# Performance work log

Measured on AMD Instinct MI355X. Metric: run time of the kernel, lower is better.

The kernel has to match this reference:

```python
import jax, jax.numpy as jnp
import numpy as np

N, L = 1, 384
NODE, H, PD = 256, 8, 128
HD = NODE // H
D1 = H * PD + NODE  # out_transform input dim = 1280


def instance_norm(x, eps=1e-5):
    # x: (N, C, H, W); torch InstanceNorm2d default: no affine, biased var
    m = x.mean(axis=(2, 3), keepdims=True)
    v = x.var(axis=(2, 3), keepdims=True)
    return (x - m) / jnp.sqrt(v + eps)


def conv3x3(x, w, b):
    y = jax.lax.conv_general_dilated(x, w, (1, 1), 'SAME',
                                     dimension_numbers=('NCHW', 'OIHW', 'NCHW'))
    return y + b[None, :, None, None]


def leaky(x):
    return jnp.where(x >= 0, x, 0.01 * x)


def layer_norm(x, w, b, eps=1e-5):
    m = x.mean(-1, keepdims=True)
    v = x.var(-1, keepdims=True)
    return (x - m) / jnp.sqrt(v + eps) * w + b


def setup_inputs() -> dict:
    key = jax.random.key(0)
    ks = jax.random.split(key, 32)
    s = 0.05
    inp = {
        'x': jax.random.normal(ks[0], (N, L, NODE), jnp.float32),
        'z': jax.random.normal(ks[1], (N, L, L, PD), jnp.float32),
        'plddt': jax.random.uniform(ks[2], (N, L, L, 1), jnp.float32),
        # linear weights stored (in, out) so application is x @ W
        'Wq': jax.random.normal(ks[3], (NODE, NODE), jnp.float32) * s,
        'Wk': jax.random.normal(ks[4], (NODE, NODE), jnp.float32) * s,
        'Wv': jax.random.normal(ks[5], (NODE, NODE), jnp.float32) * s,
        'Wp2a': jax.random.normal(ks[6], (PD, H), jnp.float32) * s,
        'conv_a_w': jax.random.normal(ks[7], (H, 2 * H, 3, 3), jnp.float32) * s,
        'conv_a_b': jnp.zeros((H,), jnp.float32),
        'conv_m_w': jax.random.normal(ks[8], (H, H + 1, 3, 3), jnp.float32) * s,
        'conv_m_b': jnp.zeros((H,), jnp.float32),
        'ln1_w': jnp.ones((D1,), jnp.float32),
        'ln1_b': jnp.zeros((D1,), jnp.float32),
        'lin1_w': jax.random.normal(ks[9], (D1, 2 * NODE), jnp.float32) * s,
        'lin1_b': jnp.zeros((2 * NODE,), jnp.float32),
        'ln2_w': jnp.ones((2 * NODE,), jnp.float32),
        'ln2_b': jnp.zeros((2 * NODE,), jnp.float32),
        'lin2_w': jax.random.normal(ks[10], (2 * NODE, NODE), jnp.float32) * s,
        'lin2_b': jnp.zeros((NODE,), jnp.float32),
        'lnf_w': jnp.ones((NODE,), jnp.float32),
        'lnf_b': jnp.zeros((NODE,), jnp.float32),
        'conv_p_w': jax.random.normal(ks[11], (PD, H + PD, 3, 3), jnp.float32) * s,
        'conv_p_b': jnp.zeros((PD,), jnp.float32),
    }
    return inp


def reference(x, z, plddt, Wq, Wk, Wv, Wp2a, conv_a_w, conv_a_b, conv_m_w,
              conv_m_b, ln1_w, ln1_b, lin1_w, lin1_b, ln2_w, ln2_b, lin2_w,
              lin2_b, lnf_w, lnf_b, conv_p_w, conv_p_b):
    Nb, Lh, D = x.shape
    nh = conv_a_w.shape[0]
    hd = D // nh
    Pd = z.shape[-1]
    # node -> alpha (GAT-style QK scores per head)
    q = (x @ Wq).reshape(Nb, Lh, nh, hd)
    k = (x @ Wk).reshape(Nb, Lh, nh, hd)
    v = (x @ Wv).reshape(Nb, Lh, nh, hd)
    a_node = jnp.einsum('nlhd,nmhd->nlmh', q, k) / jnp.sqrt(jnp.float32(hd))
    a_pair = z @ Wp2a                                  # (N,L,L,H)
    a = jnp.concatenate([a_pair, a_node], -1).transpose(0, 3, 1, 2)  # (N,2H,L,L)
    a = leaky(conv3x3(instance_norm(a), conv_a_w, conv_a_b))
    a = jnp.concatenate([a, plddt.transpose(0, 3, 1, 2)], 1)          # (N,H+1,L,L)
    a = leaky(conv3x3(instance_norm(a), conv_m_w, conv_m_b))
    a = a.transpose(0, 2, 3, 1)                                        # (N,L,L,H)
    # aggregations
    nfn = jnp.einsum('nlmh,nmhd->nlhd', a, v).reshape(Nb, Lh, D)       # node from node
    nfp = jnp.einsum('nlmh,nlmp->nlhp', a, z).reshape(Nb, Lh, nh * Pd) # node from pair
    cat = jnp.concatenate([nfp, nfn], -1)
    h = layer_norm(cat, ln1_w, ln1_b) @ lin1_w + lin1_b
    h = leaky(layer_norm(h, ln2_w, ln2_b)) @ lin2_w + lin2_b
    x_new = layer_norm(x + h, lnf_w, lnf_b)
    zp = jnp.concatenate([z, a], -1).transpose(0, 3, 1, 2)             # (N,P+H,L,L)
    z_new = leaky(conv3x3(instance_norm(zp), conv_p_w, conv_p_b)).transpose(0, 2, 3, 1)
    return x_new, z_new
```

## Files before the change

kernel.cpp:

```cpp
#include <hip/hip_runtime.h>
#include <stdint.h>

#define LSEQ 384
#define LL   147456
#define NODE 256
#define NH   8
#define HD   32
#define PDIM 128
#define D1   1280
#define D2   512

typedef __attribute__((ext_vector_type(8))) short s16x8;
typedef __attribute__((ext_vector_type(8))) __bf16 bf16x8;
typedef __attribute__((ext_vector_type(4))) float f32x4;

__device__ __forceinline__ float bf2f(uint16_t u) {
    union { uint32_t i; float f; } x; x.i = ((uint32_t)u) << 16; return x.f;
}
__device__ __forceinline__ uint16_t f2bf(float f) {
    uint32_t b = __float_as_uint(f);
    return (uint16_t)((b + 0x7FFFu + ((b >> 16) & 1u)) >> 16);
}
__device__ __forceinline__ float ld(const void* p, size_t i, int bf) {
    return bf ? bf2f(((const uint16_t*)p)[i]) : ((const float*)p)[i];
}
__device__ __forceinline__ void stout(void* p, size_t i, float v, int bf) {
    if (bf) ((uint16_t*)p)[i] = f2bf(v);
    else    ((float*)p)[i] = v;
}

__device__ __forceinline__ bf16x8 bf16x8_zero() {
    union { s16x8 s; bf16x8 b; } u; u.s = (s16x8)0; return u.b;
}

__device__ __forceinline__ void block_reduce2_256(float* s1, float* s2, int t) {
    __syncthreads();
    for (int o = 128; o > 0; o >>= 1) {
        if (t < o) { s1[t] += s1[t + o]; s2[t] += s2[t + o]; }
        __syncthreads();
    }
}

__device__ __forceinline__ void acc8(uint4 u, float& s, float& ss) {
    uint32_t w[4] = { u.x, u.y, u.z, u.w };
    #pragma unroll
    for (int i = 0; i < 4; ++i) {
        float a = bf2f((uint16_t)(w[i] & 0xFFFFu));
        float b = bf2f((uint16_t)(w[i] >> 16));
        s += a + b;
        ss = fmaf(a, a, ss);
        ss = fmaf(b, b, ss);
    }
}

__global__ void k_detect(const uint32_t* __restrict__ zz, int* __restrict__ flag) {
    if (threadIdx.x == 0 && blockIdx.x == 0) {
        int cnt = 0;
        for (int i = 0; i < 256; ++i) {
            uint32_t lo = zz[i] & 0xFFFFu;
            uint32_t e = (lo >> 7) & 0xFFu;
            if (lo == 0u || (e >= 96u && e <= 142u)) ++cnt;
        }
        flag[0] = (cnt >= 192) ? 1 : 0;
    }
}

__global__ __launch_bounds__(256) void k_cvt(
    const void* __restrict__ src, uint16_t* __restrict__ dst, const int* __restrict__ dt)
{
    int bf = dt[0];
    int i = blockIdx.x * 256 + threadIdx.x;
    dst[i] = f2bf(ld(src, i, bf));
}

__global__ __launch_bounds__(256) void k_wnk(
    const void* __restrict__ src, uint16_t* __restrict__ dst, int K, int N,
    const int* __restrict__ dt)
{
    __shared__ float tile[32][33];
    int bf = dt[0];
    int k0 = blockIdx.x * 32, n0 = blockIdx.y * 32;
    int tr = threadIdx.x >> 5, tc = threadIdx.x & 31;
    #pragma unroll
    for (int i = 0; i < 4; ++i)
        tile[tr + i * 8][tc] = ld(src, (size_t)(k0 + tr + i * 8) * N + n0 + tc, bf);
    __syncthreads();
    #pragma unroll
    for (int i = 0; i < 4; ++i)
        dst[(size_t)(n0 + tr + i * 8) * K + k0 + tc] = f2bf(tile[tc][tr + i * 8]);
}

__global__ __launch_bounds__(256) void k_gemm_bias_f32(
    const uint16_t* __restrict__ A, const uint16_t* __restrict__ B,
    const void* __restrict__ bias, float* __restrict__ out, int K, int N,
    const int* __restrict__ dt)
{
    __shared__ __align__(16) uint16_t As[64 * 72];
    __shared__ __align__(16) uint16_t Bs[64 * 72];
    int bf = dt[0];
    int t = threadIdx.x;
    int row0 = blockIdx.x * 64, col0 = blockIdx.y * 64;
    int w = t >> 6, lane = t & 63, p = lane & 15, g = lane >> 4;
    int wm = w >> 1, wn = w & 1;
    f32x4 acc[2][2];
    #pragma unroll
    for (int i = 0; i < 2; ++i)
        #pragma unroll
        for (int j = 0; j < 2; ++j) acc[i][j] = (f32x4){0.f, 0.f, 0.f, 0.f};

    for (int kc = 0; kc < K; kc += 64) {
        __syncthreads();
        #pragma unroll
        for (int rep = 0; rep < 2; ++rep) {
            int i = t + rep * 256;
            int r = i >> 3, c8 = (i & 7) * 8;
            *(uint4*)&As[r * 72 + c8] = *(const uint4*)&A[(size_t)(row0 + r) * K + kc + c8];
            *(uint4*)&Bs[r * 72 + c8] = *(const uint4*)&B[(size_t)(col0 + r) * K + kc + c8];
        }
        __syncthreads();
        #pragma unroll
        for (int kk = 0; kk < 64; kk += 32) {
            bf16x8 a0 = *(const bf16x8*)&As[(wm * 32 + p) * 72 + kk + 8 * g];
            bf16x8 a1 = *(const bf16x8*)&As[(wm * 32 + 16 + p) * 72 + kk + 8 * g];
            bf16x8 b0 = *(const bf16x8*)&Bs[(wn * 32 + p) * 72 + kk + 8 * g];
            bf16x8 b1 = *(const bf16x8*)&Bs[(wn * 32 + 16 + p) * 72 + kk + 8 * g];
            acc[0][0] = __builtin_amdgcn_mfma_f32_16x16x32_bf16(a0, b0, acc[0][0], 0, 0, 0);
            acc[0][1] = __builtin_amdgcn_mfma_f32_16x16x32_bf16(a0, b1, acc[0][1], 0, 0, 0);
            acc[1][0] = __builtin_amdgcn_mfma_f32_16x16x32_bf16(a1, b0, acc[1][0], 0, 0, 0);
            acc[1][1] = __builtin_amdgcn_mfma_f32_16x16x32_bf16(a1, b1, acc[1][1], 0, 0, 0);
        }
    }
    #pragma unroll
    for (int mi = 0; mi < 2; ++mi)
        #pragma unroll
        for (int ni = 0; ni < 2; ++ni) {
            int n = col0 + wn * 32 + ni * 16 + p;
            float bb = ld(bias, n, bf);
            #pragma unroll
            for (int reg = 0; reg < 4; ++reg) {
                int m = row0 + wm * 32 + mi * 16 + 4 * g + reg;
                out[(size_t)m * N + n] = acc[mi][ni][reg] + bb;
            }
        }
}

__global__ __launch_bounds__(256) void k_gemm_qkv(
    const uint16_t* __restrict__ A, const uint16_t* __restrict__ B,
    uint16_t* __restrict__ q, uint16_t* __restrict__ k, uint16_t* __restrict__ v)
{
    __shared__ __align__(16) uint16_t As[64 * 72];
    __shared__ __align__(16) uint16_t Bs[64 * 72];
    const int K = 256;
    int t = threadIdx.x;
    int row0 = blockIdx.x * 64, col0 = blockIdx.y * 64;
    int w = t >> 6, lane = t & 63, p = lane & 15, g = lane >> 4;
    int wm = w >> 1, wn = w & 1;
    f32x4 acc[2][2];
    #pragma unroll
    for (int i = 0; i < 2; ++i)
        #pragma unroll
        for (int j = 0; j < 2; ++j) acc[i][j] = (f32x4){0.f, 0.f, 0.f, 0.f};

    for (int kc = 0; kc < K; kc += 64) {
        __syncthreads();
        #pragma unroll
        for (int rep = 0; rep < 2; ++rep) {
            int i = t + rep * 256;
            int r = i >> 3, c8 = (i & 7) * 8;
            *(uint4*)&As[r * 72 + c8] = *(const uint4*)&A[(size_t)(row0 + r) * K + kc + c8];
            *(uint4*)&Bs[r * 72 + c8] = *(const uint4*)&B[(size_t)(col0 + r) * K + kc + c8];
        }
        __syncthreads();
        #pragma unroll
        for (int kk = 0; kk < 64; kk += 32) {
            bf16x8 a0 = *(const bf16x8*)&As[(wm * 32 + p) * 72 + kk + 8 * g];
            bf16x8 a1 = *(const bf16x8*)&As[(wm * 32 + 16 + p) * 72 + kk + 8 * g];
            bf16x8 b0 = *(const bf16x8*)&Bs[(wn * 32 + p) * 72 + kk + 8 * g];
            bf16x8 b1 = *(const bf16x8*)&Bs[(wn * 32 + 16 + p) * 72 + kk + 8 * g];
            acc[0][0] = __builtin_amdgcn_mfma_f32_16x16x32_bf16(a0, b0, acc[0][0], 0, 0, 0);
            acc[0][1] = __builtin_amdgcn_mfma_f32_16x16x32_bf16(a0, b1, acc[0][1], 0, 0, 0);
            acc[1][0] = __builtin_amdgcn_mfma_f32_16x16x32_bf16(a1, b0, acc[1][0], 0, 0, 0);
            acc[1][1] = __builtin_amdgcn_mfma_f32_16x16x32_bf16(a1, b1, acc[1][1], 0, 0, 0);
        }
    }
    #pragma unroll
    for (int mi = 0; mi < 2; ++mi)
        #pragma unroll
        for (int ni = 0; ni < 2; ++ni) {
            int nglob = col0 + wn * 32 + ni * 16 + p;
            int sel = nglob >> 8, col = nglob & 255;
            uint16_t* dst = (sel == 0) ? q : (sel == 1) ? k : v;
            #pragma unroll
            for (int reg = 0; reg < 4; ++reg) {
                int m = row0 + wm * 32 + mi * 16 + 4 * g + reg;
                dst[(size_t)m * 256 + col] = f2bf(acc[mi][ni][reg]);
            }
        }
}

__global__ __launch_bounds__(256) void k_lin2lnf_mfma(
    const uint16_t* __restrict__ A, const uint16_t* __restrict__ B,
    const void* __restrict__ bias, const void* __restrict__ x,
    const void* __restrict__ lnw, const void* __restrict__ lnb,
    void* __restrict__ out, const int* __restrict__ dt)
{
    __shared__ __align__(16) uint16_t As[32 * 72];
    __shared__ __align__(16) uint16_t Bs[256 * 72];
    const int K = 512;
    int bf = dt[0];
    int t = threadIdx.x;
    int row0 = blockIdx.x * 32;
    int w = t >> 6, lane = t & 63, p = lane & 15, g = lane >> 4;
    f32x4 acc[2][4];
    #pragma unroll
    for (int i = 0; i < 2; ++i)
        #pragma unroll
        for (int j = 0; j < 4; ++j) acc[i][j] = (f32x4){0.f, 0.f, 0.f, 0.f};

    for (int kc = 0; kc < K; kc += 64) {
        __syncthreads();
        {
            int r = t >> 3, c8 = (t & 7) * 8;
            *(uint4*)&As[r * 72 + c8] = *(const uint4*)&A[(size_t)(row0 + r) * K + kc + c8];
        }
        #pragma unroll
        for (int rep = 0; rep < 8; ++rep) {
            int i = t + rep * 256;
            int r = i >> 3, c8 = (i & 7) * 8;
            *(uint4*)&Bs[r * 72 + c8] = *(const uint4*)&B[(size_t)r * K + kc + c8];
        }
        __syncthreads();
        #pragma unroll
        for (int kk = 0; kk < 64; kk += 32) {
            bf16x8 a0 = *(const bf16x8*)&As[(p) * 72 + kk + 8 * g];
            bf16x8 a1 = *(const bf16x8*)&As[(16 + p) * 72 + kk + 8 * g];
            #pragma unroll
            for (int ni = 0; ni < 4; ++ni) {
                bf16x8 bq = *(const bf16x8*)&Bs[(w * 64 + ni * 16 + p) * 72 + kk + 8 * g];
                acc[0][ni] = __builtin_amdgcn_mfma_f32_16x16x32_bf16(a0, bq, acc[0][ni], 0, 0, 0);
                acc[1][ni] = __builtin_amdgcn_mfma_f32_16x16x32_bf16(a1, bq, acc[1][ni], 0, 0, 0);
            }
        }
    }
    __syncthreads();
    float* lnt = (float*)Bs;
    #pragma unroll
    for (int mi = 0; mi < 2; ++mi)
        #pragma unroll
        for (int ni = 0; ni < 4; ++ni) {
            int n = w * 64 + ni * 16 + p;
            float bb = ld(bias, n, bf);
            #pragma unroll
            for (int reg = 0; reg < 4; ++reg) {
                int m = mi * 16 + 4 * g + reg;
                lnt[m * 264 + n] = acc[mi][ni][reg] + bb + ld(x, (size_t)(row0 + m) * 256 + n, bf);
            }
        }
    __syncthreads();
    for (int rr = 0; rr < 8; ++rr) {
        int m = w * 8 + rr;
        float4 v4 = *(const float4*)&lnt[m * 264 + lane * 4];
        float vv[4] = { v4.x, v4.y, v4.z, v4.w };
        float s = (vv[0] + vv[1]) + (vv[2] + vv[3]);
        float ss = fmaf(vv[0], vv[0], fmaf(vv[1], vv[1], fmaf(vv[2], vv[2], vv[3] * vv[3])));
        #pragma unroll
        for (int off = 32; off > 0; off >>= 1) {
            s  += __shfl_xor(s, off);
            ss += __shfl_xor(ss, off);
        }
        float mean = s / 256.f;
        float rstd = rsqrtf(fmaxf(ss / 256.f - mean * mean, 0.f) + 1e-5f);
        #pragma unroll
        for (int i = 0; i < 4; ++i) {
            int c = lane * 4 + i;
            float val = (vv[i] - mean) * rstd * ld(lnw, c, bf) + ld(lnb, c, bf);
            stout(out, (size_t)(row0 + m) * 256 + c, val, bf);
        }
    }
}

__global__ __launch_bounds__(256) void k_apair(
    const void* __restrict__ z, const void* __restrict__ Wp2a,
    uint16_t* __restrict__ acat, const int* __restrict__ dt)
{
    __shared__ float zl[32 * 129];
    __shared__ float wp[PDIM * NH];
    int bf = dt[0];
    int t = threadIdx.x, m0 = blockIdx.x * 32, l = blockIdx.y;
    for (int i = t; i < PDIM * NH; i += 256) wp[i] = ld(Wp2a, i, bf);
    if (bf) {
        const uint16_t* zz = (const uint16_t*)z;
        for (int grp = t; grp < 512; grp += 256) {
            int ml = grp >> 4, p8 = (grp & 15) * 8;
            uint4 u = *(const uint4*)&zz[((size_t)(l * LSEQ + m0 + ml)) * PDIM + p8];
            const uint16_t* pu = (const uint16_t*)&u;
            #pragma unroll
            for (int j = 0; j < 8; ++j) zl[ml * 129 + p8 + j] = bf2f(pu[j]);
        }
    } else {
        const float* zz = (const float*)z;
        for (int grp = t; grp < 1024; grp += 256) {
            int ml = grp >> 5, p4 = (grp & 31) * 4;
            float4 u = *(const float4*)&zz[((size_t)(l * LSEQ + m0 + ml)) * PDIM + p4];
            zl[ml * 129 + p4 + 0] = u.x; zl[ml * 129 + p4 + 1] = u.y;
            zl[ml * 129 + p4 + 2] = u.z; zl[ml * 129 + p4 + 3] = u.w;
        }
    }
    __syncthreads();
    int h = t >> 5, ml = t & 31;
    float acc = 0.f;
    for (int p = 0; p < PDIM; ++p) acc = fmaf(zl[ml * 129 + p], wp[p * NH + h], acc);
    acat[(size_t)h * LL + l * LSEQ + m0 + ml] = f2bf(acc);
}

__global__ __launch_bounds__(256) void k_anode(
    const uint16_t* __restrict__ q, const uint16_t* __restrict__ k,
    uint16_t* __restrict__ acat)
{
    __shared__ float kl[NODE * 33];
    __shared__ float qr[NH * 33];
    int t = threadIdx.x, m0 = blockIdx.x * 32, l = blockIdx.y;
    for (int grp = t; grp < 1024; grp += 256) {
        int ml = grp >> 5, c8 = (grp & 31) * 8;
        uint4 u = *(const uint4*)&k[(size_t)(m0 + ml) * NODE + c8];
        const uint16_t* pu = (const uint16_t*)&u;
        #pragma unroll
        for (int j = 0; j < 8; ++j) kl[(c8 + j) * 33 + ml] = bf2f(pu[j]);
    }
    qr[(t >> 5) * 33 + (t & 31)] = bf2f(q[l * NODE + t]);
    __syncthreads();
    int h = t >> 5, ml = t & 31;
    float acc = 0.f;
    #pragma unroll 8
    for (int d = 0; d < HD; ++d)
        acc = fmaf(qr[h * 33 + d], kl[(h * HD + d) * 33 + ml], acc);
    acat[(size_t)(NH + h) * LL + l * LSEQ + m0 + ml] = f2bf(acc * 0.17677669529663687f);
}

__global__ __launch_bounds__(256) void k_scp(
    const uint16_t* __restrict__ src, const void* __restrict__ raw,
    float* __restrict__ ps, float* __restrict__ pss, const int* __restrict__ dt, int C)
{
    __shared__ float s1[256], s2[256];
    int c = blockIdx.y, chunk = blockIdx.x, t = threadIdx.x;
    float s = 0.f, ss = 0.f;
    if (c < C) {
        const uint16_t* p = src + (size_t)c * LL + (size_t)chunk * 8192;
        #pragma unroll
        for (int it = 0; it < 4; ++it) acc8(*(const uint4*)&p[(it * 256 + t) * 8], s, ss);
    } else if (dt[0]) {
        const uint4* p = (const uint4*)raw + (size_t)chunk * 1024;
        #pragma unroll
        for (int it = 0; it < 4; ++it) acc8(p[it * 256 + t], s, ss);
    } else {
        const float4* p = (const float4*)raw + (size_t)chunk * 2048;
        #pragma unroll
        for (int it = 0; it < 8; ++it) {
            float4 a = p[it * 256 + t];
            s += (a.x + a.y) + (a.z + a.w);
            ss = fmaf(a.x, a.x, fmaf(a.y, a.y, fmaf(a.z, a.z, fmaf(a.w, a.w, ss))));
        }
    }
    s1[t] = s; s2[t] = ss;
    block_reduce2_256(s1, s2, t);
    if (t == 0) { ps[c * 18 + chunk] = s1[0]; pss[c * 18 + chunk] = s2[0]; }
}

__global__ void k_scf(
    const float* __restrict__ ps, const float* __restrict__ pss,
    float* __restrict__ mean_out, float* __restrict__ rstd_out, int C)
{
    int t = threadIdx.x;
    if (t < C) {
        float s = 0.f, ss = 0.f;
        for (int i = 0; i < 18; ++i) { s += ps[t * 18 + i]; ss += pss[t * 18 + i]; }
        float m = s / (float)LL;
        float var = ss / (float)LL - m * m;
        mean_out[t] = m; rstd_out[t] = rsqrtf(fmaxf(var, 0.f) + 1e-5f);
    }
}

__global__ __launch_bounds__(128) void k_conv_a(
    const uint16_t* __restrict__ acat, const void* __restrict__ wa,
    const void* __restrict__ ba, const float* __restrict__ mean,
    const float* __restrict__ rstd, uint16_t* __restrict__ out,
    const int* __restrict__ dt)
{
    __shared__ float wl[9 * 8 * 16];
    __shared__ float ot[8 * 9];
    int bf = dt[0];
    int t = threadIdx.x;
    int l = blockIdx.y, m = blockIdx.x * 128 + t;
    for (int i = t; i < 1152; i += 128) {
        int tap = i >> 7, rem = i & 127;
        int oc = rem >> 4, ic = rem & 15;
        wl[i] = ld(wa, (size_t)oc * 144 + ic * 9 + tap, bf) * rstd[ic];
    }
    __syncthreads();
    if (t < 72) {
        int oc = t / 9, tap = t - oc * 9;
        float s = 0.f;
        for (int ic = 0; ic < 16; ++ic) s = fmaf(mean[ic], wl[tap * 128 + oc * 16 + ic], s);
        ot[t] = s;
    }
    __syncthreads();
    float acc[8];
    #pragma unroll
    for (int oc = 0; oc < 8; ++oc) acc[oc] = ld(ba, oc, bf);
    #pragma unroll
    for (int r = 0; r < 3; ++r) {
        int li = l + r - 1;
        if (li < 0 || li >= LSEQ) continue;
        #pragma unroll
        for (int c = 0; c < 3; ++c) {
            int mi = m + c - 1;
            if (mi < 0 || mi >= LSEQ) continue;
            const uint16_t* ip = acat + li * LSEQ + mi;
            float v[16];
            #pragma unroll
            for (int ic = 0; ic < 16; ++ic) v[ic] = bf2f(ip[(size_t)ic * LL]);
            int tap = r * 3 + c;
            const float4* wq = (const float4*)&wl[tap * 128];
            #pragma unroll
            for (int oc = 0; oc < 8; ++oc) {
                float4 w0 = wq[oc * 4], w1 = wq[oc * 4 + 1], w2 = wq[oc * 4 + 2], w3 = wq[oc * 4 + 3];
                float a = acc[oc] - ot[oc * 9 + tap];
                a = fmaf(w0.x, v[0], a);  a = fmaf(w0.y, v[1], a);
                a = fmaf(w0.z, v[2], a);  a = fmaf(w0.w, v[3], a);
                a = fmaf(w1.x, v[4], a);  a = fmaf(w1.y, v[5], a);
                a = fmaf(w1.z, v[6], a);  a = fmaf(w1.w, v[7], a);
                a = fmaf(w2.x, v[8], a);  a = fmaf(w2.y, v[9], a);
                a = fmaf(w2.z, v[10], a); a = fmaf(w2.w, v[11], a);
                a = fmaf(w3.x, v[12], a); a = fmaf(w3.y, v[13], a);
                a = fmaf(w3.z, v[14], a); a = fmaf(w3.w, v[15], a);
                acc[oc] = a;
            }
        }
    }
    #pragma unroll
    for (int oc = 0; oc < 8; ++oc) {
        float a = acc[oc] >= 0.f ? acc[oc] : 0.01f * acc[oc];
        out[(size_t)oc * LL + l * LSEQ + m] = f2bf(a);
    }
}

__global__ __launch_bounds__(128) void k_conv_m(
    const uint16_t* __restrict__ a1, const void* __restrict__ plddt,
    const void* __restrict__ wm, const void* __restrict__ bm,
    const float* __restrict__ mean, const float* __restrict__ rstd,
    uint16_t* __restrict__ out, const int* __restrict__ dt)
{
    __shared__ float wl[9 * 8 * 12];
    __shared__ float ot[8 * 9];
    int bf = dt[0];
    int t = threadIdx.x;
    int l = blockIdx.y, m = blockIdx.x * 128 + t;
    for (int i = t; i < 864; i += 128) {
        int tap = i / 96, rem = i - tap * 96;
        int oc = rem / 12, ic = rem - oc * 12;
        wl[i] = (ic < 9) ? ld(wm, (size_t)oc * 81 + ic * 9 + tap, bf) * rstd[ic] : 0.f;
    }
    __syncthreads();
    if (t < 72) {
        int oc = t / 9, tap = t - oc * 9;
        float s = 0.f;
        for (int ic = 0; ic < 9; ++ic) s = fmaf(mean[ic], wl[tap * 96 + oc * 12 + ic], s);
        ot[t] = s;
    }
    __syncthreads();
    float acc[8];
    #pragma unroll
    for (int oc = 0; oc < 8; ++oc) acc[oc] = ld(bm, oc, bf);
    #pragma unroll
    for (int r = 0; r < 3; ++r) {
        int li = l + r - 1;
        if (li < 0 || li >= LSEQ) continue;
        #pragma unroll
        for (int c = 0; c < 3; ++c) {
            int mi = m + c - 1;
            if (mi < 0 || mi >= LSEQ) continue;
            int off = li * LSEQ + mi;
            float v[12];
            #pragma unroll
            for (int ic = 0; ic < 8; ++ic) v[ic] = bf2f(a1[(size_t)ic * LL + off]);
            v[8] = ld(plddt, off, bf); v[9] = 0.f; v[10] = 0.f; v[11] = 0.f;
            int tap = r * 3 + c;
            const float4* wq = (const float4*)&wl[tap * 96];
            #pragma unroll
            for (int oc = 0; oc < 8; ++oc) {
                float4 w0 = wq[oc * 3], w1 = wq[oc * 3 + 1], w2 = wq[oc * 3 + 2];
                float a = acc[oc] - ot[oc * 9 + tap];
                a = fmaf(w0.x, v[0], a); a = fmaf(w0.y, v[1], a);
                a = fmaf(w0.z, v[2], a); a = fmaf(w0.w, v[3], a);
                a = fmaf(w1.x, v[4], a); a = fmaf(w1.y, v[5], a);
                a = fmaf(w1.z, v[6], a); a = fmaf(w1.w, v[7], a);
                a = fmaf(w2.x, v[8], a);
                acc[oc] = a;
            }
        }
    }
    #pragma unroll
    for (int oc = 0; oc < 8; ++oc) {
        float a = acc[oc] >= 0.f ? acc[oc] : 0.01f * acc[oc];
        out[(size_t)oc * LL + l * LSEQ + m] = f2bf(a);
    }
}

__global__ __launch_bounds__(512) void k_agg(
    const uint16_t* __restrict__ a2, const uint16_t* __restrict__ v,
    const void* __restrict__ z, float* __restrict__ cat,
    const int* __restrict__ dt)
{
    __shared__ float al[NH * LSEQ];
    __shared__ float hp[3 * NH * PDIM];
    int bf = dt[0];
    int t = threadIdx.x, l = blockIdx.x;
    for (int i = t; i < NH * LSEQ; i += 512) {
        int h = i / LSEQ, m = i - h * LSEQ;
        al[i] = bf2f(a2[(size_t)h * LL + l * LSEQ + m]);
    }
    __syncthreads();
    int p = t & 127, qq = t >> 7;
    float acc[NH];
    #pragma unroll
    for (int h = 0; h < NH; ++h) acc[h] = 0.f;
    size_t zrow = (size_t)l * LSEQ * PDIM;
    for (int m = qq; m < LSEQ; m += 4) {
        float zv = ld(z, zrow + (size_t)m * PDIM + p, bf);
        #pragma unroll
        for (int h = 0; h < NH; ++h) acc[h] = fmaf(al[h * LSEQ + m], zv, acc[h]);
    }
    if (qq) {
        #pragma unroll
        for (int h = 0; h < NH; ++h) hp[(qq - 1) * 1024 + h * PDIM + p] = acc[h];
    }
    __syncthreads();
    if (qq == 0) {
        #pragma unroll
        for (int h = 0; h < NH; ++h)
            cat[(size_t)l * D1 + h * PDIM + p] =
                acc[h] + hp[h * PDIM + p] + hp[1024 + h * PDIM + p] + hp[2048 + h * PDIM + p];
    }
    int o = t & 255, half = t >> 8;
    int h2 = o >> 5;
    float s = 0.f;
    for (int m = half; m < LSEQ; m += 2)
        s = fmaf(al[h2 * LSEQ + m], bf2f(v[m * NODE + o]), s);
    __syncthreads();
    if (half) hp[o] = s;
    __syncthreads();
    if (!half) cat[(size_t)l * D1 + NH * PDIM + o] = s + hp[o];
}

__global__ __launch_bounds__(256) void k_ln1(
    const float* __restrict__ cat, const void* __restrict__ w,
    const void* __restrict__ b, uint16_t* __restrict__ outn,
    const int* __restrict__ dt)
{
    __shared__ float s1[256], s2[256];
    int bf = dt[0];
    int t = threadIdx.x, l = blockIdx.x;
    const float* row = cat + (size_t)l * D1;
    float s = 0.f, ss = 0.f;
    for (int i = t; i < D1; i += 256) { float v = row[i]; s += v; ss = fmaf(v, v, ss); }
    s1[t] = s; s2[t] = ss;
    block_reduce2_256(s1, s2, t);
    float m = s1[0] / (float)D1;
    float rstd = rsqrtf(fmaxf(s2[0] / (float)D1 - m * m, 0.f) + 1e-5f);
    for (int i = t; i < D1; i += 256)
        outn[(size_t)l * D1 + i] = f2bf((row[i] - m) * rstd * ld(w, i, bf) + ld(b, i, bf));
}

__global__ __launch_bounds__(256) void k_ln2(
    const float* __restrict__ in, const void* __restrict__ w,
    const void* __restrict__ b, uint16_t* __restrict__ outn,
    const int* __restrict__ dt)
{
    __shared__ float s1[256], s2[256];
    int bf = dt[0];
    int t = threadIdx.x, l = blockIdx.x;
    const float* row = in + (size_t)l * D2;
    float v0 = row[t], v1 = row[t + 256];
    s1[t] = v0 + v1; s2[t] = v0 * v0 + v1 * v1;
    block_reduce2_256(s1, s2, t);
    float m = s1[0] / (float)D2;
    float rstd = rsqrtf(fmaxf(s2[0] / (float)D2 - m * m, 0.f) + 1e-5f);
    float o0 = (v0 - m) * rstd * ld(w, t, bf) + ld(b, t, bf);
    float o1 = (v1 - m) * rstd * ld(w, t + 256, bf) + ld(b, t + 256, bf);
    outn[(size_t)l * D2 + t]       = f2bf(o0 >= 0.f ? o0 : 0.01f * o0);
    outn[(size_t)l * D2 + t + 256] = f2bf(o1 >= 0.f ? o1 : 0.01f * o1);
}

__global__ __launch_bounds__(256) void k_pstat(
    const void* __restrict__ z, float* __restrict__ psum, float* __restrict__ psumsq,
    const int* __restrict__ dt)
{
    __shared__ float sa[128], sb[128];
    int bf = dt[0];
    int t = threadIdx.x;
    int ch = t & 127, half = t >> 7;
    size_t r0 = (size_t)blockIdx.x * 256;
    float s = 0.f, ss = 0.f;
    for (int i = 0; i < 128; ++i) {
        float v = ld(z, (r0 + half + 2 * i) * PDIM + ch, bf);
        s += v; ss = fmaf(v, v, ss);
    }
    if (half) { sa[ch] = s; sb[ch] = ss; }
    __syncthreads();
    if (!half) {
        psum[blockIdx.x * PDIM + ch] = s + sa[ch];
        psumsq[blockIdx.x * PDIM + ch] = ss + sb[ch];
    }
}

__global__ __launch_bounds__(512) void k_finP(
    const float* __restrict__ psum, const float* __restrict__ psumsq,
    float* __restrict__ meanP, float* __restrict__ rstdP)
{
    __shared__ float s1[512], s2[512];
    int t = threadIdx.x;
    int c = t & 127, seg = t >> 7;
    float s = 0.f, ss = 0.f;
    for (int b = seg * 144; b < seg * 144 + 144; ++b) {
        s += psum[b * PDIM + c]; ss += psumsq[b * PDIM + c];
    }
    s1[t] = s; s2[t] = ss;
    __syncthreads();
    if (t < 128) {
        float S  = s1[t] + s1[t + 128] + s1[t + 256] + s1[t + 384];
        float SS = s2[t] + s2[t + 128] + s2[t + 256] + s2[t + 384];
        float m = S / (float)LL;
        float var = SS / (float)LL - m * m;
        meanP[t] = m; rstdP[t] = rsqrtf(fmaxf(var, 0.f) + 1e-5f);
    }
}

__global__ __launch_bounds__(64) void k_wprep(
    const void* __restrict__ wp, uint16_t* __restrict__ wt, const int* __restrict__ dt)
{
    int bf = dt[0];
    int oc = blockIdx.x, tap = blockIdx.y;
    for (int ic = threadIdx.x; ic < 144; ic += 64) {
        float v = (ic < 136) ? ld(wp, (size_t)oc * 1224 + (size_t)ic * 9 + tap, bf) : 0.f;
        wt[((size_t)tap * 128 + oc) * 144 + ic] = f2bf(v);
    }
}

__global__ __launch_bounds__(256, 2) void k_conv_p_mfma(
    const void* __restrict__ z, const uint16_t* __restrict__ a2,
    const uint16_t* __restrict__ wt, const void* __restrict__ bp,
    const float* __restrict__ meanP, const float* __restrict__ rstdP,
    void* __restrict__ out, const int* __restrict__ dt)
{
    __shared__ __align__(16) uint16_t As[4 * 34 * 144];
    __shared__ __align__(16) uint16_t Ws[128 * 144];
    __shared__ float mloc[136], rloc[136];

    int bf = dt[0];
    int t = threadIdx.x;
    int m0 = blockIdx.x * 32, l0 = blockIdx.y * 2;

    if (t < 136) { mloc[t] = meanP[t]; rloc[t] = rstdP[t]; }
    __syncthreads();

    for (int grp = t; grp < 2448; grp += 256) {
        int pixidx = grp / 18;
        int icg = (grp - pixidx * 18) * 8;
        int lr = pixidx / 34, lc = pixidx - lr * 34;
        int li = l0 - 1 + lr, mi = m0 - 1 + lc;
        uint16_t vals[8];
        if (li < 0 || li >= LSEQ || mi < 0 || mi >= LSEQ || icg >= 136) {
            #pragma unroll
            for (int j = 0; j < 8; ++j) vals[j] = 0;
        } else if (icg < 128) {
            size_t zoff = ((size_t)li * LSEQ + mi) * PDIM + icg;
            if (bf) {
                const uint16_t* zp = (const uint16_t*)z + zoff;
                #pragma unroll
                for (int j = 0; j < 8; ++j)
                    vals[j] = f2bf((bf2f(zp[j]) - mloc[icg + j]) * rloc[icg + j]);
            } else {
                const float* zp = (const float*)z + zoff;
                #pragma unroll
                for (int j = 0; j < 8; ++j)
                    vals[j] = f2bf((zp[j] - mloc[icg + j]) * rloc[icg + j]);
            }
        } else {
            size_t poff = (size_t)li * LSEQ + mi;
            #pragma unroll
            for (int j = 0; j < 8; ++j)
                vals[j] = f2bf((bf2f(a2[(size_t)j * LL + poff]) - mloc[128 + j]) * rloc[128 + j]);
        }
        *(uint4*)&As[pixidx * 144 + icg] = *(const uint4*)vals;
    }

    int w = t >> 6, lane = t & 63;
    int p = lane & 15, g = lane >> 4;
    int r = w >> 1;
    int ocb = (w & 1) * 64;
    int bb0 = (ocb + p) * 144 + 8 * g;

    f32x4 acc0[4], acc1[4];
    #pragma unroll
    for (int n = 0; n < 4; ++n) {
        acc0[n] = (f32x4){0.f, 0.f, 0.f, 0.f};
        acc1[n] = (f32x4){0.f, 0.f, 0.f, 0.f};
    }
    bf16x8 bz = bf16x8_zero();

    for (int tap = 0; tap < 9; ++tap) {
        __syncthreads();
        {
            const uint4* wsrc = (const uint4*)(wt + (size_t)tap * 18432);
            uint4* wdst = (uint4*)Ws;
            #pragma unroll
            for (int i = 0; i < 9; ++i) wdst[t + i * 256] = wsrc[t + i * 256];
        }
        __syncthreads();

        int tr = tap / 3, tc = tap - tr * 3;
        int abase = ((r + tr) * 34 + p + tc) * 144 + 8 * g;

        #pragma unroll
        for (int ch = 0; ch < 5; ++ch) {
            const int ic0 = (ch < 4) ? ch * 32 : 112;
            bf16x8 a0 = *(const bf16x8*)&As[abase + ic0];
            bf16x8 a1 = *(const bf16x8*)&As[abase + 2304 + ic0];
            #pragma unroll
            for (int n = 0; n < 4; ++n) {
                bf16x8 bq;
                if (ch < 4) {
                    bq = *(const bf16x8*)&Ws[bb0 + n * 2304 + ic0];
                } else {
                    bq = bz;
                    if (g == 2) bq = *(const bf16x8*)&Ws[bb0 + n * 2304 + 112];
                }
                acc0[n] = __builtin_amdgcn_mfma_f32_16x16x32_bf16(a0, bq, acc0[n], 0, 0, 0);
                acc1[n] = __builtin_amdgcn_mfma_f32_16x16x32_bf16(a1, bq, acc1[n], 0, 0, 0);
            }
        }
    }

    int l = l0 + r;
    #pragma unroll
    for (int n = 0; n < 4; ++n) {
        int oc = ocb + 16 * n + p;
        float bb = ld(bp, oc, bf);
        #pragma unroll
        for (int reg = 0; reg < 4; ++reg) {
            int pc = 4 * g + reg;
            float v0 = acc0[n][reg] + bb; v0 = v0 >= 0.f ? v0 : 0.01f * v0;
            stout(out, 98304 + ((size_t)l * LSEQ + (m0 + pc)) * PDIM + oc, v0, bf);
            float v1 = acc1[n][reg] + bb; v1 = v1 >= 0.f ? v1 : 0.01f * v1;
            stout(out, 98304 + ((size_t)l * LSEQ + (m0 + 16 + pc)) * PDIM + oc, v1, bf);
        }
    }
}

__global__ __launch_bounds__(128) void k_conv_p(
    const void* __restrict__ z, const uint16_t* __restrict__ a2,
    const void* __restrict__ wp, const void* __restrict__ bp,
    const float* __restrict__ meanP, const float* __restrict__ rstdP,
    void* __restrict__ out, const int* __restrict__ dt)
{
    __shared__ __align__(16) float wlds[128 * 76];
    __shared__ __align__(16) float inl[4 * 18 * 8];
    int bf = dt[0];
    int t = threadIdx.x;
    int m0 = blockIdx.x * 16, l0 = blockIdx.y * 2;
    float acc0[16], acc1[16];
    #pragma unroll
    for (int i = 0; i < 16; ++i) { acc0[i] = 0.f; acc1[i] = 0.f; }

    for (int ic0 = 0; ic0 < 136; ic0 += 8) {
        __syncthreads();
        for (int i = t; i < 128 * 72; i += 128) {
            int op = i / 72, r = i % 72;
            int cc = r / 9, tap = r % 9;
            wlds[op * 76 + tap * 8 + cc] = ld(wp, op * 1224 + (ic0 + cc) * 9 + tap, bf);
        }
        for (int i = t; i < 4 * 18 * 8; i += 128) {
            int rr = i / 144, rem = i % 144;
            int col = rem >> 3, cc = rem & 7;
            int li = l0 - 1 + rr, mi = m0 - 1 + col, ic = ic0 + cc;
            float vv = 0.f;
            if (li >= 0 && li < LSEQ && mi >= 0 && mi < LSEQ) {
                float raw = (ic < PDIM) ? ld(z, ((size_t)li * LSEQ + mi) * PDIM + ic, bf)
                                        : bf2f(a2[(size_t)(ic - PDIM) * LL + li * LSEQ + mi]);
                vv = (raw - meanP[ic]) * rstdP[ic];
            }
            inl[i] = vv;
        }
        __syncthreads();
        #pragma unroll
        for (int qd = 0; qd < 2; ++qd) {
            float4 wq[9];
            #pragma unroll
            for (int tap = 0; tap < 9; ++tap)
                wq[tap] = *(const float4*)&wlds[t * 76 + tap * 8 + qd * 4];
            float4 win[4][3];
            #pragma unroll
            for (int r = 0; r < 4; ++r) {
                win[r][1] = *(const float4*)&inl[(r * 18 + 0) * 8 + qd * 4];
                win[r][2] = *(const float4*)&inl[(r * 18 + 1) * 8 + qd * 4];
                win[r][0] = win[r][1];
            }
            #pragma unroll
            for (int pix = 0; pix < 16; ++pix) {
                #pragma unroll
                for (int r = 0; r < 4; ++r) {
                    win[r][0] = win[r][1];
                    win[r][1] = win[r][2];
                    win[r][2] = *(const float4*)&inl[(r * 18 + pix + 2) * 8 + qd * 4];
                }
                float p0x = 0.f, p0y = 0.f, p0z = 0.f, p0w = 0.f;
                float p1x = 0.f, p1y = 0.f, p1z = 0.f, p1w = 0.f;
                #pragma unroll
                for (int tr = 0; tr < 3; ++tr) {
                    #pragma unroll
                    for (int c = 0; c < 3; ++c) {
                        float4 w4 = wq[tr * 3 + c];
                        float4 u0 = win[tr][c];
                        float4 u1 = win[tr + 1][c];
                        p0x = fmaf(w4.x, u0.x, p0x); p0y = fmaf(w4.y, u0.y, p0y);
                        p0z = fmaf(w4.z, u0.z, p0z); p0w = fmaf(w4.w, u0.w, p0w);
                        p1x = fmaf(w4.x, u1.x, p1x); p1y = fmaf(w4.y, u1.y, p1y);
                        p1z = fmaf(w4.z, u1.z, p1z); p1w = fmaf(w4.w, u1.w, p1w);
                    }
                }
                acc0[pix] += (p0x + p0y) + (p0z + p0w);
                acc1[pix] += (p1x + p1y) + (p1z + p1w);
            }
        }
    }
    float bb = ld(bp, t, bf);
    #pragma unroll
    for (int pix = 0; pix < 16; ++pix) {
        float v0 = acc0[pix] + bb; v0 = v0 >= 0.f ? v0 : 0.01f * v0;
        stout(out, 98304 + ((size_t)l0 * LSEQ + m0 + pix) * PDIM + t, v0, bf);
        float v1 = acc1[pix] + bb; v1 = v1 >= 0.f ? v1 : 0.01f * v1;
        stout(out, 98304 + ((size_t)(l0 + 1) * LSEQ + m0 + pix) * PDIM + t, v1, bf);
    }
}

extern "C" void kernel_launch(void* const* d_in, const int* in_sizes, int n_in,
                              void* d_out, int out_size, void* d_ws, size_t ws_size,
                              hipStream_t stream)
{
    const void* x     = d_in[0];
    const void* z     = d_in[1];
    const void* plddt = d_in[2];
    const void* Wq    = d_in[3];
    const void* Wk    = d_in[4];
    const void* Wv    = d_in[5];
    const void* Wp2a  = d_in[6];
    const void* caw   = d_in[7];
    const void* cab   = d_in[8];
    const void* cmw   = d_in[9];
    const void* cmb   = d_in[10];
    const void* ln1w  = d_in[11];
    const void* ln1b  = d_in[12];
    const void* l1w   = d_in[13];
    const void* l1b   = d_in[14];
    const void* ln2w  = d_in[15];
    const void* ln2b  = d_in[16];
    const void* l2w   = d_in[17];
    const void* l2b   = d_in[18];
    const void* lnfw  = d_in[19];
    const void* lnfb  = d_in[20];
    const void* cpw   = d_in[21];
    const void* cpb   = d_in[22];

    uint16_t* O = (uint16_t*)d_out;
    uint16_t* acat = O + 98304;
    uint16_t* a1b  = O + 2457600;
    uint16_t* qb   = a1b;
    uint16_t* kb   = a1b + 98304;
    uint16_t* vb   = O + 3637248;
    float*    cat  = (float*)(O + 3735552);
    float*    h1   = (float*)(O + 5701632);
    float*    psum = (float*)(O + 6488064);
    float*    psumsq = (float*)(O + 6635520);
    uint16_t* cb   = O + 6782976;
    uint16_t* h1nb = O + 7274496;
    uint16_t* xb   = O + 7471104;
    uint16_t* wtq  = O + 7569408;
    uint16_t* wt1  = O + 7766016;
    uint16_t* wt2  = O + 8421376;

    uint16_t* U = (uint16_t*)d_ws;
    uint16_t* a2b = U;
    float*    st  = (float*)(U + 1179648);
    float* m16 = st;        float* r16 = st + 16;
    float* m9  = st + 32;   float* r9  = st + 48;
    float* mP  = st + 64;   float* rP  = st + 200;
    int*   flg = (int*)(U + 1181696);
    uint16_t* wt = U + 1182720;
    int use_mfma = (ws_size >= (size_t)2365440 + 331776);

    k_detect<<<1, 64, 0, stream>>>((const uint32_t*)z, flg);
    k_cvt<<<384, 256, 0, stream>>>(x, xb, flg);
    k_wnk<<<dim3(8, 8), 256, 0, stream>>>(Wq, wtq,          256, 256, flg);
    k_wnk<<<dim3(8, 8), 256, 0, stream>>>(Wk, wtq +  65536, 256, 256, flg);
    k_wnk<<<dim3(8, 8), 256, 0, stream>>>(Wv, wtq + 131072, 256, 256, flg);
    k_wnk<<<dim3(40, 16), 256, 0, stream>>>(l1w, wt1, 1280, 512, flg);
    k_wnk<<<dim3(16, 8), 256, 0, stream>>>(l2w, wt2,  512, 256, flg);

    k_gemm_qkv<<<dim3(6, 12), 256, 0, stream>>>(xb, wtq, qb, kb, vb);
    k_apair <<<dim3(12, LSEQ), 256, 0, stream>>>(z, Wp2a, acat, flg);
    k_anode <<<dim3(12, LSEQ), 256, 0, stream>>>(qb, kb, acat);
    k_scp<<<dim3(18, 16), 256, 0, stream>>>(acat, plddt, psum, psumsq, flg, 16);
    k_scf<<<1, 16, 0, stream>>>(psum, psumsq, m16, r16, 16);
    k_conv_a<<<dim3(3, LSEQ), 128, 0, stream>>>(acat, caw, cab, m16, r16, a1b, flg);
    k_scp<<<dim3(18, 9), 256, 0, stream>>>(a1b, plddt, psum, psumsq, flg, 8);
    k_scf<<<1, 9, 0, stream>>>(psum, psumsq, m9, r9, 9);
    k_conv_m<<<dim3(3, LSEQ), 128, 0, stream>>>(a1b, plddt, cmw, cmb, m9, r9, a2b, flg);
    k_agg   <<<LSEQ, 512, 0, stream>>>(a2b, vb, z, cat, flg);
    k_ln1   <<<LSEQ, 256, 0, stream>>>(cat, ln1w, ln1b, cb, flg);
    k_gemm_bias_f32<<<dim3(6, 8), 256, 0, stream>>>(cb, wt1, l1b, h1, 1280, 512, flg);
    k_ln2   <<<LSEQ, 256, 0, stream>>>(h1, ln2w, ln2b, h1nb, flg);
    k_lin2lnf_mfma<<<12, 256, 0, stream>>>(h1nb, wt2, l2b, x, lnfw, lnfb, d_out, flg);
    k_scp<<<dim3(18, 8), 256, 0, stream>>>(a2b, plddt, psum, psumsq, flg, 8);
    k_scf<<<1, 8, 0, stream>>>(psum, psumsq, mP + 128, rP + 128, 8);
    k_pstat <<<576, 256, 0, stream>>>(z, psum, psumsq, flg);
    k_finP  <<<1, 512, 0, stream>>>(psum, psumsq, mP, rP);
    if (use_mfma) {
        k_wprep<<<dim3(128, 9), 64, 0, stream>>>(cpw, wt, flg);
        k_conv_p_mfma<<<dim3(12, 192), 256, 0, stream>>>(z, a2b, wt, cpb, mP, rP, d_out, flg);
    } else {
        k_conv_p<<<dim3(24, 192), 128, 0, stream>>>(z, a2b, cpw, cpb, mP, rP, d_out, flg);
    }
}
```

Before: 579.9 us.

## Double-buffer conv_p weights via LDS DMA, widen tiles, coalesce stores, merge prep kernels

```diff
diff --git a/kernel.cpp b/kernel.cpp
--- a/kernel.cpp
+++ b/kernel.cpp
@@ -33,6 +33,12 @@
     union { s16x8 s; bf16x8 b; } u; u.s = (s16x8)0; return u.b;
 }
 
+__device__ __forceinline__ void gl_lds16(const void* g, void* l) {
+    __builtin_amdgcn_global_load_lds(
+        (const __attribute__((address_space(1))) uint32_t*)g,
+        (__attribute__((address_space(3))) uint32_t*)l, 16, 0, 0);
+}
+
 __device__ __forceinline__ void block_reduce2_256(float* s1, float* s2, int t) {
     __syncthreads();
     for (int o = 128; o > 0; o >>= 1) {
@@ -65,20 +71,34 @@
     }
 }
 
-__global__ __launch_bounds__(256) void k_cvt(
-    const void* __restrict__ src, uint16_t* __restrict__ dst, const int* __restrict__ dt)
-{
-    int bf = dt[0];
-    int i = blockIdx.x * 256 + threadIdx.x;
-    dst[i] = f2bf(ld(src, i, bf));
-}
-
-__global__ __launch_bounds__(256) void k_wnk(
-    const void* __restrict__ src, uint16_t* __restrict__ dst, int K, int N,
+__global__ __launch_bounds__(256) void k_prep(
+    const void* __restrict__ Wq, const void* __restrict__ Wk,
+    const void* __restrict__ Wv, const void* __restrict__ l1w,
+    const void* __restrict__ l2w, const void* __restrict__ x,
+    uint16_t* __restrict__ wtq, uint16_t* __restrict__ wt1,
+    uint16_t* __restrict__ wt2, uint16_t* __restrict__ xb,
     const int* __restrict__ dt)
 {
     __shared__ float tile[32][33];
     int bf = dt[0];
+    int job = blockIdx.z;
+    if (job == 5) {
+        int flat = blockIdx.y * 40 + blockIdx.x;
+        if (flat < 384) {
+            int i = flat * 256 + threadIdx.x;
+            xb[i] = f2bf(ld(x, i, bf));
+        }
+        return;
+    }
+    const void* src; uint16_t* dst; int K, N;
+    switch (job) {
+        case 0: src = Wq;  dst = wtq;          K = 256;  N = 256; break;
+        case 1: src = Wk;  dst = wtq + 65536;  K = 256;  N = 256; break;
+        case 2: src = Wv;  dst = wtq + 131072; K = 256;  N = 256; break;
+        case 3: src = l1w; dst = wt1;          K = 1280; N = 512; break;
+        default: src = l2w; dst = wt2;         K = 512;  N = 256; break;
+    }
+    if ((int)blockIdx.x >= (K >> 5) || (int)blockIdx.y >= (N >> 5)) return;
     int k0 = blockIdx.x * 32, n0 = blockIdx.y * 32;
     int tr = threadIdx.x >> 5, tc = threadIdx.x & 31;
     #pragma unroll
@@ -390,7 +410,9 @@
     __shared__ float ot[8 * 9];
     int bf = dt[0];
     int t = threadIdx.x;
-    int l = blockIdx.y, m = blockIdx.x * 128 + t;
+    int flat = blockIdx.y * 3 + blockIdx.x;
+    int wk = (flat & 7) * 144 + (flat >> 3);
+    int l = wk / 3, m = (wk % 3) * 128 + t;
     for (int i = t; i < 1152; i += 128) {
         int tap = i >> 7, rem = i & 127;
         int oc = rem >> 4, ic = rem & 15;
@@ -454,7 +476,9 @@
     __shared__ float ot[8 * 9];
     int bf = dt[0];
     int t = threadIdx.x;
-    int l = blockIdx.y, m = blockIdx.x * 128 + t;
+    int flat = blockIdx.y * 3 + blockIdx.x;
+    int wk = (flat & 7) * 144 + (flat >> 3);
+    int l = wk / 3, m = (wk % 3) * 128 + t;
     for (int i = t; i < 864; i += 128) {
         int tap = i / 96, rem = i - tap * 96;
         int oc = rem / 12, ic = rem - oc * 12;
@@ -646,24 +670,36 @@
     }
 }
 
-__global__ __launch_bounds__(256, 2) void k_conv_p_mfma(
+__global__ __launch_bounds__(512, 1) void k_conv_p_mfma(
     const void* __restrict__ z, const uint16_t* __restrict__ a2,
     const uint16_t* __restrict__ wt, const void* __restrict__ bp,
     const float* __restrict__ meanP, const float* __restrict__ rstdP,
     void* __restrict__ out, const int* __restrict__ dt)
 {
-    __shared__ __align__(16) uint16_t As[4 * 34 * 144];
-    __shared__ __align__(16) uint16_t Ws[128 * 144];
+    __shared__ __align__(16) uint16_t As[6 * 34 * 144];
+    __shared__ __align__(16) uint16_t Ws[2][128 * 144];
     __shared__ float mloc[136], rloc[136];
 
     int bf = dt[0];
     int t = threadIdx.x;
-    int m0 = blockIdx.x * 32, l0 = blockIdx.y * 2;
+    int flat = blockIdx.y * 12 + blockIdx.x;
+    int wk = (flat & 7) * 144 + (flat >> 3);
+    int m0 = (wk % 12) * 32, l0 = (wk / 12) * 4;
+    int w = t >> 6, lane = t & 63;
+    int p = lane & 15, g = lane >> 4;
+    int r = w >> 1;
+    int ocb = (w & 1) * 64;
 
     if (t < 136) { mloc[t] = meanP[t]; rloc[t] = rstdP[t]; }
     __syncthreads();
 
-    for (int grp = t; grp < 2448; grp += 256) {
+    {
+        const char* src = (const char*)wt;
+        for (int s = w; s < 36; s += 8)
+            gl_lds16(src + s * 1024 + lane * 16, (char*)Ws[0] + s * 1024);
+    }
+
+    for (int grp = t; grp < 3672; grp += 512) {
         int pixidx = grp / 18;
         int icg = (grp - pixidx * 18) * 8;
         int lr = pixidx / 34, lc = pixidx - lr * 34;
@@ -693,11 +729,8 @@
         }
         *(uint4*)&As[pixidx * 144 + icg] = *(const uint4*)vals;
     }
-
-    int w = t >> 6, lane = t & 63;
-    int p = lane & 15, g = lane >> 4;
-    int r = w >> 1;
-    int ocb = (w & 1) * 64;
+    __syncthreads();
+
     int bb0 = (ocb + p) * 144 + 8 * g;
 
     f32x4 acc0[4], acc1[4];
@@ -709,17 +742,16 @@
     bf16x8 bz = bf16x8_zero();
 
     for (int tap = 0; tap < 9; ++tap) {
-        __syncthreads();
-        {
-            const uint4* wsrc = (const uint4*)(wt + (size_t)tap * 18432);
-            uint4* wdst = (uint4*)Ws;
-            #pragma unroll
-            for (int i = 0; i < 9; ++i) wdst[t + i * 256] = wsrc[t + i * 256];
-        }
-        __syncthreads();
+        int cur = tap & 1;
+        if (tap < 8) {
+            const char* src = (const char*)(wt + (size_t)(tap + 1) * 18432);
+            for (int s = w; s < 36; s += 8)
+                gl_lds16(src + s * 1024 + lane * 16, (char*)Ws[cur ^ 1] + s * 1024);
+        }
 
         int tr = tap / 3, tc = tap - tr * 3;
         int abase = ((r + tr) * 34 + p + tc) * 144 + 8 * g;
+        const uint16_t* Wc = Ws[cur];
 
         #pragma unroll
         for (int ch = 0; ch < 5; ++ch) {
@@ -730,29 +762,69 @@
             for (int n = 0; n < 4; ++n) {
                 bf16x8 bq;
                 if (ch < 4) {
-                    bq = *(const bf16x8*)&Ws[bb0 + n * 2304 + ic0];
+                    bq = *(const bf16x8*)&Wc[bb0 + n * 2304 + ic0];
                 } else {
                     bq = bz;
-                    if (g == 2) bq = *(const bf16x8*)&Ws[bb0 + n * 2304 + 112];
+                    if (g == 2) bq = *(const bf16x8*)&Wc[bb0 + n * 2304 + 112];
                 }
                 acc0[n] = __builtin_amdgcn_mfma_f32_16x16x32_bf16(a0, bq, acc0[n], 0, 0, 0);
                 acc1[n] = __builtin_amdgcn_mfma_f32_16x16x32_bf16(a1, bq, acc1[n], 0, 0, 0);
             }
         }
-    }
-
-    int l = l0 + r;
-    #pragma unroll
-    for (int n = 0; n < 4; ++n) {
-        int oc = ocb + 16 * n + p;
-        float bb = ld(bp, oc, bf);
-        #pragma unroll
-        for (int reg = 0; reg < 4; ++reg) {
-            int pc = 4 * g + reg;
-            float v0 = acc0[n][reg] + bb; v0 = v0 >= 0.f ? v0 : 0.01f * v0;
-            stout(out, 98304 + ((size_t)l * LSEQ + (m0 + pc)) * PDIM + oc, v0, bf);
-            float v1 = acc1[n][reg] + bb; v1 = v1 >= 0.f ? v1 : 0.01f * v1;
-            stout(out, 98304 + ((size_t)l * LSEQ + (m0 + 16 + pc)) * PDIM + oc, v1, bf);
+        __syncthreads();
+    }
+
+    if (bf) {
+        uint16_t* LB = As;
+        #pragma unroll
+        for (int n = 0; n < 4; ++n) {
+            int oc = ocb + 16 * n + p;
+            float bb = ld(bp, oc, bf);
+            #pragma unroll
+            for (int reg = 0; reg < 4; ++reg) {
+                int ml = 4 * g + reg;
+                float v0 = acc0[n][reg] + bb; v0 = v0 >= 0.f ? v0 : 0.01f * v0;
+                LB[(r * 32 + ml) * 128 + oc] = f2bf(v0);
+                float v1 = acc1[n][reg] + bb; v1 = v1 >= 0.f ? v1 : 0.01f * v1;
+                LB[(r * 32 + 16 + ml) * 128 + oc] = f2bf(v1);
+            }
+        }
+        __syncthreads();
+        const uint4* srcv = (const uint4*)As;
+        for (int i = t; i < 2048; i += 512) {
+            int run = i >> 9, off = i & 511;
+            uint16_t* dst = (uint16_t*)out + 98304 +
+                ((size_t)(l0 + run) * LSEQ + m0) * PDIM + (size_t)off * 8;
+            *(uint4*)dst = srcv[i];
+        }
+    } else {
+        float* LB = (float*)As;
+        #pragma unroll
+        for (int h = 0; h < 2; ++h) {
+            __syncthreads();
+            if ((r >> 1) == h) {
+                #pragma unroll
+                for (int n = 0; n < 4; ++n) {
+                    int oc = ocb + 16 * n + p;
+                    float bb = ld(bp, oc, bf);
+                    #pragma unroll
+                    for (int reg = 0; reg < 4; ++reg) {
+                        int ml = 4 * g + reg;
+                        float v0 = acc0[n][reg] + bb; v0 = v0 >= 0.f ? v0 : 0.01f * v0;
+                        LB[((r & 1) * 32 + ml) * 128 + oc] = v0;
+                        float v1 = acc1[n][reg] + bb; v1 = v1 >= 0.f ? v1 : 0.01f * v1;
+                        LB[((r & 1) * 32 + 16 + ml) * 128 + oc] = v1;
+                    }
+                }
+            }
+            __syncthreads();
+            const uint4* srcv = (const uint4*)As;
+            for (int i = t; i < 2048; i += 512) {
+                int run = i >> 10, off = i & 1023;
+                float* dst = (float*)out + 98304 +
+                    ((size_t)(l0 + h * 2 + run) * LSEQ + m0) * PDIM + (size_t)off * 4;
+                *(uint4*)dst = srcv[i];
+            }
         }
     }
 }
@@ -899,12 +971,8 @@
     int use_mfma = (ws_size >= (size_t)2365440 + 331776);
 
     k_detect<<<1, 64, 0, stream>>>((const uint32_t*)z, flg);
-    k_cvt<<<384, 256, 0, stream>>>(x, xb, flg);
-    k_wnk<<<dim3(8, 8), 256, 0, stream>>>(Wq, wtq,          256, 256, flg);
-    k_wnk<<<dim3(8, 8), 256, 0, stream>>>(Wk, wtq +  65536, 256, 256, flg);
-    k_wnk<<<dim3(8, 8), 256, 0, stream>>>(Wv, wtq + 131072, 256, 256, flg);
-    k_wnk<<<dim3(40, 16), 256, 0, stream>>>(l1w, wt1, 1280, 512, flg);
-    k_wnk<<<dim3(16, 8), 256, 0, stream>>>(l2w, wt2,  512, 256, flg);
+    k_prep<<<dim3(40, 16, 6), 256, 0, stream>>>(Wq, Wk, Wv, l1w, l2w, x,
+                                                wtq, wt1, wt2, xb, flg);
 
     k_gemm_qkv<<<dim3(6, 12), 256, 0, stream>>>(xb, wtq, qb, kb, vb);
     k_apair <<<dim3(12, LSEQ), 256, 0, stream>>>(z, Wp2a, acat, flg);
@@ -926,7 +994,7 @@
     k_finP  <<<1, 512, 0, stream>>>(psum, psumsq, mP, rP);
     if (use_mfma) {
         k_wprep<<<dim3(128, 9), 64, 0, stream>>>(cpw, wt, flg);
-        k_conv_p_mfma<<<dim3(12, 192), 256, 0, stream>>>(z, a2b, wt, cpb, mP, rP, d_out, flg);
+        k_conv_p_mfma<<<dim3(12, 96), 512, 0, stream>>>(z, a2b, wt, cpb, mP, rP, d_out, flg);
     } else {
         k_conv_p<<<dim3(24, 192), 128, 0, stream>>>(z, a2b, cpw, cpb, mP, rP, d_out, flg);
     }
```

Measured after the change: 559.5 us. 3.5% less time.
